# Performance work log

Measured on AMD Instinct MI355X. Metric: run time of the kernel, lower is better.

The kernel has to match this reference:

```python
import jax, jax.numpy as jnp
import numpy as np

B, C, P, T, H = 4, 256, 1024, 64, 8
D = C // H
SCALE = float(np.sqrt(D * T))


def setup_inputs() -> dict:
    key = jax.random.key(0)
    ks = jax.random.split(key, 7)
    s = 1.0 / np.sqrt(C)
    return {
        "x": jax.random.normal(ks[0], (B, C, P, T), dtype=jnp.float32),
        "Wk": jax.random.uniform(ks[1], (C, C), dtype=jnp.float32, minval=-s, maxval=s),
        "bk": jax.random.uniform(ks[2], (C,), dtype=jnp.float32, minval=-s, maxval=s),
        "Wq": jax.random.uniform(ks[3], (C, C), dtype=jnp.float32, minval=-s, maxval=s),
        "bq": jax.random.uniform(ks[4], (C,), dtype=jnp.float32, minval=-s, maxval=s),
        "Wv": jax.random.uniform(ks[5], (C, C), dtype=jnp.float32, minval=-s, maxval=s),
        "bv": jax.random.uniform(ks[6], (C,), dtype=jnp.float32, minval=-s, maxval=s),
    }


def _proj_split(x, W, b):
    # 1x1 conv == channel-mixing linear; then split heads: b (h d) p t -> b h d p t
    y = jnp.einsum('bcpt,oc->bopt', x, W) + b[None, :, None, None]
    Bs, _, Ps, Ts = y.shape
    return y.reshape(Bs, H, D, Ps, Ts)


def reference(x, Wk, bk, Wq, bq, Wv, bv):
    k = _proj_split(x, Wk, bk)
    q = _proj_split(x, Wq, bq)
    v = _proj_split(x, Wv, bv)
    # contract jointly over d and t
    energy = jnp.einsum('bhdpt,bhdqt->bhpq', k, q)
    attn = jax.nn.softmax(energy / SCALE, axis=-1)
    out = jnp.einsum('bhpq,bhdpt->bhdqt', attn, v)
    # merge heads: b h d q t -> b (h d) q t
    return out.reshape(B, C, P, T)
```

## Files before the change

### kernel.cpp

```cpp
#include <hip/hip_runtime.h>
#include <cstdint>
#include <cstddef>

#define NB 4
#define NC 256
#define NP 1024
#define NT 64
#define NH 8
#define ND 32
#define NF 2048
#define NPT 65536
#define KQV_ELEMS 67108864ull
#define INV_SCALE 0.022097086912079608f

typedef unsigned short u16;
typedef __bf16 bf16x8 __attribute__((ext_vector_type(8)));
typedef short  s16x8  __attribute__((ext_vector_type(8)));
typedef short  s16x4  __attribute__((ext_vector_type(4)));
typedef float  f32x4  __attribute__((ext_vector_type(4)));

__device__ __forceinline__ u16 f2bf(float f) {
  unsigned u = __builtin_bit_cast(unsigned, f);
  u += 0x7fffu + ((u >> 16) & 1u);
  return (u16)(u >> 16);
}
__device__ __forceinline__ float bf2f(u16 h) {
  unsigned u = ((unsigned)h) << 16;
  return __builtin_bit_cast(float, u);
}
__device__ __forceinline__ int swz(int row) { return ((row ^ (row >> 3)) & 7) << 4; }

#define GLOAD_LDS16(gp, lp) __builtin_amdgcn_global_load_lds( \
    (const __attribute__((address_space(1))) void*)(gp),      \
    (__attribute__((address_space(3))) void*)(lp), 16, 0, 0)

__device__ __forceinline__ f32x4 mfma16(bf16x8 a, bf16x8 b, f32x4 c) {
  return __builtin_amdgcn_mfma_f32_16x16x32_bf16(a, b, c, 0, 0, 0);
}

__global__ __launch_bounds__(256) void wcast_kernel(
    const float* __restrict__ Wk, const float* __restrict__ Wq,
    const float* __restrict__ Wv, u16* __restrict__ wbf)
{
  int pj = blockIdx.y;
  const float* W = (pj == 0) ? Wk : ((pj == 1) ? Wq : Wv);
  int idx = blockIdx.x * 1024 + threadIdx.x * 4;
  float4 v = *(const float4*)(W + idx);
  s16x4 pk;
  pk[0] = (short)f2bf(v.x); pk[1] = (short)f2bf(v.y);
  pk[2] = (short)f2bf(v.z); pk[3] = (short)f2bf(v.w);
  *(s16x4*)(wbf + (size_t)pj * 65536 + idx) = pk;
}

__global__ __launch_bounds__(256, 2) void xcast_kernel(
    const float* __restrict__ x, u16* __restrict__ xT)
{
  int ptt = blockIdx.x;
  int ct  = blockIdx.y;
  int b   = blockIdx.z;
  __shared__ __align__(16) u16 L[64 * 64];
  int tid = threadIdx.x;
#pragma unroll
  for (int i = 0; i < 4; i++) {
    int cl  = i * 16 + (tid >> 4);
    int ptl = (tid & 15) * 4;
    float4 v = *(const float4*)(x + ((size_t)(b * NC + ct * 64 + cl)) * NPT +
                                ptt * 64 + ptl);
    s16x4 pk;
    pk[0] = (short)f2bf(v.x); pk[1] = (short)f2bf(v.y);
    pk[2] = (short)f2bf(v.z); pk[3] = (short)f2bf(v.w);
    *(s16x4*)((char*)L + ((cl * 128 + ptl * 2) ^ swz(cl))) = pk;
  }
  __syncthreads();
#pragma unroll
  for (int i = 0; i < 2; i++) {
    int ptl = i * 32 + (tid >> 3);
    int c8  = (tid & 7) * 8;
    s16x8 v;
#pragma unroll
    for (int j = 0; j < 8; j++) {
      int row = c8 + j;
      v[j] = (short)*(const u16*)((char*)L + ((row * 128 + ptl * 2) ^ swz(row)));
    }
    *(s16x8*)(xT + ((size_t)b * NPT + (size_t)ptt * 64 + ptl) * NC + ct * 64 + c8) = v;
  }
}

template <int KT>
__device__ __forceinline__ void gemm_core(const u16* __restrict__ A,
                                          const u16* __restrict__ Bp,
                                          u16* As, u16* Bs, f32x4 acc[4][4])
{
  const int tid = threadIdx.x, lane = tid & 63, wave = tid >> 6;
  const int wm = (wave >> 1) * 64, wn = (wave & 1) * 64;
  for (int ks = 0; ks < KT / 64; ks++) {
    const int k0 = ks * 64;
    __syncthreads();
#pragma unroll
    for (int i = 0; i < 4; i++) {
      int r0 = wave * 32 + i * 8;
      int row = r0 + (lane >> 3);
      int col = k0 + (lane & 7) * 8;
      GLOAD_LDS16(A  + (size_t)row * KT + col, &As[r0 * 64]);
      GLOAD_LDS16(Bp + (size_t)row * KT + col, &Bs[r0 * 64]);
    }
    __syncthreads();
#pragma unroll
    for (int kk = 0; kk < 2; kk++) {
      bf16x8 af[4], bfr[4];
#pragma unroll
      for (int f = 0; f < 4; f++) {
        int ra = wm + f * 16 + (lane & 15);
        af[f]  = *(const bf16x8*)((char*)As + ra * 128 + kk * 64 + (lane >> 4) * 16);
        int rb = wn + f * 16 + (lane & 15);
        bfr[f] = *(const bf16x8*)((char*)Bs + rb * 128 + kk * 64 + (lane >> 4) * 16);
      }
#pragma unroll
      for (int fm = 0; fm < 4; fm++)
#pragma unroll
        for (int fn = 0; fn < 4; fn++)
          acc[fm][fn] = mfma16(af[fm], bfr[fn], acc[fm][fn]);
    }
  }
}

__global__ __launch_bounds__(256, 2) void proj_kernel(
    const u16* __restrict__ wbf, const u16* __restrict__ xT,
    const float* __restrict__ bk, const float* __restrict__ bq,
    const float* __restrict__ bv, u16* __restrict__ kqv)
{
  int d0 = blockIdx.x;
  int b  = blockIdx.y;
  int xcd = d0 & 7, r = d0 >> 3;
  int j = r % 6, tch = r / 6;
  int ptile = tch * 8 + xcd;
  int pj = j >> 1, mt = j & 1;
  const float* bias = (pj == 0) ? bk : ((pj == 1) ? bq : bv);
  u16* outb = kqv + (size_t)pj * KQV_ELEMS;

  const int m0 = mt * 128;
  const int n0 = ptile * 128;

  const u16* A  = wbf + (size_t)pj * 65536 + (size_t)m0 * NC;
  const u16* Bp = xT + ((size_t)b * NPT + (size_t)n0) * NC;

  __shared__ __align__(16) u16 As[128 * 64];
  __shared__ __align__(16) u16 Bs[128 * 64];

  f32x4 acc[4][4];
#pragma unroll
  for (int a = 0; a < 4; a++)
#pragma unroll
    for (int c = 0; c < 4; c++) acc[a][c] = (f32x4){0.f, 0.f, 0.f, 0.f};

  gemm_core<NC>(A, Bp, As, Bs, acc);

  const int lane = threadIdx.x & 63, wave = threadIdx.x >> 6;
  const int wm = (wave >> 1) * 64, wn = (wave & 1) * 64;
#pragma unroll
  for (int fm = 0; fm < 4; fm++) {
#pragma unroll
    for (int jj = 0; jj < 4; jj++) {
      int m = wm + fm * 16 + (lane >> 4) * 4 + jj;
      int o = m0 + m;
      float bsv = bias[o];
      int hh = o >> 5, dd = o & 31;
#pragma unroll
      for (int fn = 0; fn < 4; fn++) {
        int n = n0 + wn + fn * 16 + (lane & 15);
        int p = n >> 6, t = n & 63;
        outb[((size_t)(b * NH + hh) * NP + p) * NF + dd * 64 + t] =
            f2bf(acc[fm][fn][jj] + bsv);
      }
    }
  }
}

__global__ __launch_bounds__(256, 2) void transpose_kernel(
    const u16* __restrict__ in, u16* __restrict__ outp)
{
  int ft = blockIdx.x;
  int pt = blockIdx.y;
  int slab = blockIdx.z;
  __shared__ __align__(16) u16 L[64 * 64];
  int t = threadIdx.x;
  const u16* ip = in + (size_t)slab * NP * NF;
#pragma unroll
  for (int i = 0; i < 2; i++) {
    int pl = i * 32 + (t >> 3);
    int c8 = (t & 7) * 8;
    s16x8 v = *(const s16x8*)(ip + (size_t)(pt * 64 + pl) * NF + ft * 64 + c8);
    *(s16x8*)((char*)L + ((pl * 128 + c8 * 2) ^ swz(pl))) = v;
  }
  __syncthreads();
  u16* op = outp + (size_t)slab * NP * NF;
#pragma unroll
  for (int i = 0; i < 2; i++) {
    int fl = i * 32 + (t >> 3);
    int p8 = (t & 7) * 8;
    s16x8 v;
#pragma unroll
    for (int j2 = 0; j2 < 8; j2++) {
      int row = p8 + j2;
      v[j2] = (short)*(const u16*)((char*)L + ((row * 128 + fl * 2) ^ swz(row)));
    }
    *(s16x8*)(op + (size_t)(ft * 64 + fl) * NP + pt * 64 + p8) = v;
  }
}

__global__ __launch_bounds__(256, 2) void qk_kernel(
    const u16* __restrict__ kb, const u16* __restrict__ qb, u16* __restrict__ S)
{
  int bid = blockIdx.x;
  int xcd = bid & 7, r = bid >> 3;
  int bh = xcd * 4 + (r >> 6);
  int idx = r & 63;
  int mt = idx >> 3, nt = idx & 7;

  const u16* A  = qb + (size_t)bh * NP * NF + (size_t)mt * 128 * NF;
  const u16* Bp = kb + (size_t)bh * NP * NF + (size_t)nt * 128 * NF;

  __shared__ __align__(16) u16 As[128 * 64];
  __shared__ __align__(16) u16 Bs[128 * 64];

  f32x4 acc[4][4];
#pragma unroll
  for (int a = 0; a < 4; a++)
#pragma unroll
    for (int c = 0; c < 4; c++) acc[a][c] = (f32x4){0.f, 0.f, 0.f, 0.f};

  gemm_core<NF>(A, Bp, As, Bs, acc);

  const int lane = threadIdx.x & 63, wave = threadIdx.x >> 6;
  const int wm = (wave >> 1) * 64, wn = (wave & 1) * 64;
  u16* Sp = S + (size_t)bh * NP * NP;
#pragma unroll
  for (int fm = 0; fm < 4; fm++)
#pragma unroll
    for (int jj = 0; jj < 4; jj++) {
      int m = mt * 128 + wm + fm * 16 + (lane >> 4) * 4 + jj;
#pragma unroll
      for (int fn = 0; fn < 4; fn++) {
        int n = nt * 128 + wn + fn * 16 + (lane & 15);
        Sp[(size_t)m * NP + n] = f2bf(acc[fm][fn][jj] * INV_SCALE);
      }
    }
}

__global__ __launch_bounds__(256, 2) void softmax_kernel(
    const u16* __restrict__ S, u16* __restrict__ A)
{
  int cb = blockIdx.x;
  int bh = blockIdx.y;
  int tid = threadIdx.x;
  int c  = tid & 63;
  int qs = tid >> 6;
  int col = cb * 64 + c;
  const u16* Sp = S + (size_t)bh * NP * NP + col;
  float m = -1e30f, l = 0.f;
  for (int q = qs * 256; q < qs * 256 + 256; q++) {
    float v = bf2f(Sp[(size_t)q * NP]);
    float mn = fmaxf(m, v);
    l = l * __expf(m - mn) + __expf(v - mn);
    m = mn;
  }
  __shared__ float ms[4][64], ls[4][64];
  ms[qs][c] = m; ls[qs][c] = l;
  __syncthreads();
  float M = fmaxf(fmaxf(ms[0][c], ms[1][c]), fmaxf(ms[2][c], ms[3][c]));
  float L = ls[0][c] * __expf(ms[0][c] - M) + ls[1][c] * __expf(ms[1][c] - M) +
            ls[2][c] * __expf(ms[2][c] - M) + ls[3][c] * __expf(ms[3][c] - M);
  float inv = 1.f / L;
  u16* Ap = A + (size_t)bh * NP * NP + col;
  for (int q = qs * 256; q < qs * 256 + 256; q++) {
    float v = bf2f(Sp[(size_t)q * NP]);
    Ap[(size_t)q * NP] = f2bf(__expf(v - M) * inv);
  }
}

__global__ __launch_bounds__(256, 2) void av_kernel(
    const u16* __restrict__ Ab, const u16* __restrict__ Vt, float* __restrict__ out)
{
  int bid = blockIdx.x;
  int xcd = bid & 7, r = bid >> 3;
  int bh = xcd * 4 + (r >> 7);
  int idx = r & 127;
  int mt = idx >> 4, nt = idx & 15;

  const u16* A  = Ab + (size_t)bh * NP * NP + (size_t)mt * 128 * NP;
  const u16* Bp = Vt + (size_t)bh * NF * NP + (size_t)nt * 128 * NP;

  __shared__ __align__(16) u16 As[128 * 64];
  __shared__ __align__(16) u16 Bs[128 * 64];

  f32x4 acc[4][4];
#pragma unroll
  for (int a = 0; a < 4; a++)
#pragma unroll
    for (int c = 0; c < 4; c++) acc[a][c] = (f32x4){0.f, 0.f, 0.f, 0.f};

  gemm_core<NP>(A, Bp, As, Bs, acc);

  const int lane = threadIdx.x & 63, wave = threadIdx.x >> 6;
  const int wm = (wave >> 1) * 64, wn = (wave & 1) * 64;
  int b = bh >> 3, h = bh & 7;
#pragma unroll
  for (int fm = 0; fm < 4; fm++)
#pragma unroll
    for (int jj = 0; jj < 4; jj++) {
      int m = mt * 128 + wm + fm * 16 + (lane >> 4) * 4 + jj;
#pragma unroll
      for (int fn = 0; fn < 4; fn++) {
        int n = nt * 128 + wn + fn * 16 + (lane & 15);
        int dd = n >> 6, t = n & 63;
        out[((size_t)(b * NC + h * ND + dd) * NP + m) * NT + t] = acc[fm][fn][jj];
      }
    }
}

extern "C" void kernel_launch(void* const* d_in, const int* in_sizes, int n_in,
                              void* d_out, int out_size, void* d_ws, size_t ws_size,
                              hipStream_t stream)
{
  if (ws_size < 4ull * KQV_ELEMS * sizeof(u16)) return;

  const float* x  = (const float*)d_in[0];
  const float* Wk = (const float*)d_in[1];
  const float* bk = (const float*)d_in[2];
  const float* Wq = (const float*)d_in[3];
  const float* bq = (const float*)d_in[4];
  const float* Wv = (const float*)d_in[5];
  const float* bv = (const float*)d_in[6];

  u16* kb = (u16*)d_ws;
  u16* qb = kb + KQV_ELEMS;
  u16* vb = kb + 2 * KQV_ELEMS;
  u16* vt = kb + 3 * KQV_ELEMS;

  u16* xT  = (u16*)d_out;
  u16* wbf = xT + KQV_ELEMS;
  u16* Sb  = xT + KQV_ELEMS + 262144;
  u16* Ab  = kb;

  wcast_kernel<<<dim3(64, 3), 256, 0, stream>>>(Wk, Wq, Wv, wbf);
  xcast_kernel<<<dim3(1024, 4, 4), 256, 0, stream>>>(x, xT);
  proj_kernel<<<dim3(3072, 4), 256, 0, stream>>>(wbf, xT, bk, bq, bv, kb);
  transpose_kernel<<<dim3(32, 16, 32), 256, 0, stream>>>(vb, vt);
  qk_kernel<<<dim3(2048), 256, 0, stream>>>(kb, qb, Sb);
  softmax_kernel<<<dim3(16, 32), 256, 0, stream>>>(Sb, Ab);
  av_kernel<<<dim3(4096), 256, 0, stream>>>(Ab, vt, (float*)d_out);
}
```

Baseline: 765.2 us.

## Double-buffer LDS tiles in projection GEMM to overlap loads with MFMA

Replaces the shared gemm_core call in the QKV projection kernel with an inlined K loop that uses two LDS buffers per operand. The next 64-wide K slice is issued via direct global-to-LDS loads while MFMAs run on the current slice, with explicit vmcnt waits and barriers. This aims to hide global load latency behind compute, at the cost of doubling the LDS footprint to 64 KB, which may reduce occupancy.

```diff
diff --git a/kernel.cpp b/kernel.cpp
--- a/kernel.cpp
+++ b/kernel.cpp
@@ -144,8 +144,13 @@
   const u16* A  = wbf + (size_t)pj * 65536 + (size_t)m0 * NC;
   const u16* Bp = xT + ((size_t)b * NPT + (size_t)n0) * NC;
 
-  __shared__ __align__(16) u16 As[128 * 64];
-  __shared__ __align__(16) u16 Bs[128 * 64];
+  __shared__ __align__(16) u16 As[2][128 * 64];
+  __shared__ __align__(16) u16 Bs[2][128 * 64];
+
+  const int tid  = threadIdx.x;
+  const int lane = tid & 63;
+  const int wave = tid >> 6;
+  const int wm = (wave >> 1) * 64, wn = (wave & 1) * 64;
 
   f32x4 acc[4][4];
 #pragma unroll
@@ -153,10 +158,54 @@
 #pragma unroll
     for (int c = 0; c < 4; c++) acc[a][c] = (f32x4){0.f, 0.f, 0.f, 0.f};
 
-  gemm_core<NC>(A, Bp, As, Bs, acc);
-
-  const int lane = threadIdx.x & 63, wave = threadIdx.x >> 6;
-  const int wm = (wave >> 1) * 64, wn = (wave & 1) * 64;
+  auto STAGE = [&](int pb, int k0) {
+#pragma unroll
+    for (int i = 0; i < 4; i++) {
+      int r0 = wave * 32 + i * 8;
+      int row = r0 + (lane >> 3);
+      int col = k0 + (lane & 7) * 8;
+      GLOAD_LDS16(A  + (size_t)row * NC + col, &As[pb][r0 * 64]);
+      GLOAD_LDS16(Bp + (size_t)row * NC + col, &Bs[pb][r0 * 64]);
+    }
+  };
+
+  STAGE(0, 0);
+  __builtin_amdgcn_sched_barrier(0);
+#pragma unroll
+  for (int ks = 0; ks < 4; ks++) {
+    if (ks < 3) {
+      STAGE((ks + 1) & 1, (ks + 1) * 64);
+      __builtin_amdgcn_sched_barrier(0);
+      asm volatile("s_waitcnt vmcnt(8)" ::: "memory");
+    } else {
+      asm volatile("s_waitcnt vmcnt(0)" ::: "memory");
+    }
+    __builtin_amdgcn_s_barrier();
+    __builtin_amdgcn_sched_barrier(0);
+    const u16* Asb = As[ks & 1];
+    const u16* Bsb = Bs[ks & 1];
+#pragma unroll
+    for (int kk = 0; kk < 2; kk++) {
+      bf16x8 af[4], bfr[4];
+#pragma unroll
+      for (int f = 0; f < 4; f++) {
+        int ra = wm + f * 16 + (lane & 15);
+        af[f]  = *(const bf16x8*)((char*)Asb + ra * 128 + kk * 64 + (lane >> 4) * 16);
+        int rb = wn + f * 16 + (lane & 15);
+        bfr[f] = *(const bf16x8*)((char*)Bsb + rb * 128 + kk * 64 + (lane >> 4) * 16);
+      }
+#pragma unroll
+      for (int fm = 0; fm < 4; fm++)
+#pragma unroll
+        for (int fn = 0; fn < 4; fn++)
+          acc[fm][fn] = mfma16(af[fm], bfr[fn], acc[fm][fn]);
+    }
+    __builtin_amdgcn_sched_barrier(0);
+    asm volatile("s_waitcnt lgkmcnt(0)" ::: "memory");
+    __builtin_amdgcn_s_barrier();
+    __builtin_amdgcn_sched_barrier(0);
+  }
+
 #pragma unroll
   for (int fm = 0; fm < 4; fm++) {
 #pragma unroll
```

Result: slower. 814.2 us (+6.4%).

## Replace QK and AV GEMMs with 256x256-tile, 4-stage pipelined 512-thread kernels

Applied to the files above, without the earlier changes.

Swaps the 128x128-tile QK^T and attn·V GEMM kernels for a new core that computes 256x256 tiles with 8 waves. Operands are staged through a 4-deep ring of LDS buffers using direct global-to-LDS loads, explicit vmcnt waits and barriers, and raised wave priority around the MFMA blocks. The larger tiles are meant to cut global/L2 traffic per FLOP, and the deeper prefetch is meant to hide memory latency. The cost is 128 KB of dynamic LDS per block, much higher register pressure from 32 accumulators per thread, and fewer blocks per CU.

```diff
diff --git a/kernel.cpp b/kernel.cpp
--- a/kernel.cpp
+++ b/kernel.cpp
@@ -208,41 +208,176 @@
   }
 }
 
-__global__ __launch_bounds__(256, 2) void qk_kernel(
+#define STG1(TT, I, OP) do {                                                   \
+    const u16* gp_ = (OP ? Bg : Ag) + (size_t)grow[I] * KT + (TT) * 32 + gcol[I]; \
+    GLOAD_LDS16(gp_, L + ((((TT) & 3) * 32768 + (OP) * 16384 +                 \
+                           ((I) & 1 ? W1 : W0)) >> 1));                        \
+  } while (0)
+
+#define FENCE() do {                                                           \
+    asm volatile("" ::: "memory");                                             \
+    __builtin_amdgcn_sched_barrier(0);                                         \
+  } while (0)
+
+#define KBODY(J, WAITASM, DOSTG) do {                                          \
+    const int bufb_ = ((J) & 3) * 32768;                                       \
+    bf16x8 a_[4], b_[4];                                                       \
+    _Pragma("unroll")                                                          \
+    for (int mf = 0; mf < 4; mf++)                                             \
+      a_[mf] = *(const bf16x8*)((const char*)L + bufb_ + baseA + mf * 1024);   \
+    _Pragma("unroll")                                                          \
+    for (int nf = 0; nf < 4; nf++)                                             \
+      b_[nf] = *(const bf16x8*)((const char*)L + bufb_ + baseB + nf * 1024);   \
+    if (DOSTG) { STG1((J) + 3, 0, 0); STG1((J) + 3, 1, 0); }                   \
+    __builtin_amdgcn_s_barrier();                                              \
+    asm volatile("s_waitcnt lgkmcnt(0)" ::: "memory");                         \
+    __builtin_amdgcn_sched_barrier(0);                                         \
+    __builtin_amdgcn_s_setprio(1);                                             \
+    _Pragma("unroll")                                                          \
+    for (int mf = 0; mf < 4; mf++)                                             \
+      _Pragma("unroll")                                                        \
+      for (int nf = 0; nf < 4; nf++)                                           \
+        acc[mf][nf] = mfma16(a_[mf], b_[nf], acc[mf][nf]);                     \
+    __builtin_amdgcn_s_setprio(0);                                             \
+    __builtin_amdgcn_sched_barrier(0);                                         \
+    __builtin_amdgcn_s_barrier();                                              \
+    FENCE();                                                                   \
+    bf16x8 a2_[4];                                                             \
+    _Pragma("unroll")                                                          \
+    for (int mf = 0; mf < 4; mf++)                                             \
+      a2_[mf] = *(const bf16x8*)((const char*)L + bufb_ + baseA +              \
+                                 (4 + mf) * 1024);                             \
+    if (DOSTG) { STG1((J) + 3, 2, 1); STG1((J) + 3, 3, 1); }                   \
+    __builtin_amdgcn_s_barrier();                                              \
+    asm volatile("s_waitcnt lgkmcnt(0)" ::: "memory");                         \
+    __builtin_amdgcn_sched_barrier(0);                                         \
+    __builtin_amdgcn_s_setprio(1);                                             \
+    _Pragma("unroll")                                                          \
+    for (int mf = 0; mf < 4; mf++)                                             \
+      _Pragma("unroll")                                                        \
+      for (int nf = 0; nf < 4; nf++)                                           \
+        acc[4 + mf][nf] = mfma16(a2_[mf], b_[nf], acc[4 + mf][nf]);            \
+    __builtin_amdgcn_s_setprio(0);                                             \
+    __builtin_amdgcn_sched_barrier(0);                                         \
+    asm volatile(WAITASM ::: "memory");                                        \
+    __builtin_amdgcn_s_barrier();                                              \
+    FENCE();                                                                   \
+  } while (0)
+
+template <int KT>
+__device__ __forceinline__ void core256(const u16* __restrict__ Ag,
+                                        const u16* __restrict__ Bg,
+                                        u16* L, f32x4 acc[8][4])
+{
+  constexpr int NKT = KT / 32;
+  const int tid  = threadIdx.x;
+  const int lane = tid & 63;
+  const int wv   = tid >> 6;
+  const int wr = wv >> 2, wc = wv & 3;
+
+  int grow[4], gcol[4];
+#pragma unroll
+  for (int i = 0; i < 4; i++) {
+    int oi   = (tid + (i & 1) * 512) * 16;
+    int loff = oi ^ (((oi >> 6) & 3) << 4);
+    grow[i] = loff >> 6;
+    gcol[i] = (loff & 63) >> 1;
+  }
+  const int W0 = wv * 1024;
+  const int W1 = wv * 1024 + 8192;
+
+  const int rowA  = wr * 128 + (lane & 15);
+  const int baseA = rowA * 64 + (((lane >> 4) * 16) ^ ((rowA & 3) << 4));
+  const int rowB  = wc * 64 + (lane & 15);
+  const int baseB = 16384 + rowB * 64 + (((lane >> 4) * 16) ^ ((rowB & 3) << 4));
+
+#pragma unroll
+  for (int tt = 0; tt < 3; tt++) {
+    STG1(tt, 0, 0); STG1(tt, 1, 0); STG1(tt, 2, 1); STG1(tt, 3, 1);
+  }
+  __builtin_amdgcn_sched_barrier(0);
+  asm volatile("s_waitcnt vmcnt(8)" ::: "memory");
+  __builtin_amdgcn_s_barrier();
+  FENCE();
+
+  for (int j = 0; j < NKT - 3; ++j)
+    KBODY(j, "s_waitcnt vmcnt(8)", 1);
+  KBODY(NKT - 3, "s_waitcnt vmcnt(4)", 0);
+  KBODY(NKT - 2, "s_waitcnt vmcnt(0)", 0);
+  KBODY(NKT - 1, "", 0);
+}
+
+__global__ __launch_bounds__(512, 2) void qk256_kernel(
     const u16* __restrict__ kb, const u16* __restrict__ qb, u16* __restrict__ S)
 {
+  extern __shared__ u16 L[];
   int bid = blockIdx.x;
   int xcd = bid & 7, r = bid >> 3;
-  int bh = xcd * 4 + (r >> 6);
-  int idx = r & 63;
-  int mt = idx >> 3, nt = idx & 7;
-
-  const u16* A  = qb + (size_t)bh * NP * NF + (size_t)mt * 128 * NF;
-  const u16* Bp = kb + (size_t)bh * NP * NF + (size_t)nt * 128 * NF;
-
-  __shared__ __align__(16) u16 As[128 * 64];
-  __shared__ __align__(16) u16 Bs[128 * 64];
-
-  f32x4 acc[4][4];
-#pragma unroll
-  for (int a = 0; a < 4; a++)
+  int bh  = xcd * 4 + (r >> 4);
+  int til = r & 15;
+  int mt  = til >> 2, nt = til & 3;
+
+  const u16* Ag = qb + (size_t)bh * NP * NF + (size_t)mt * 256 * NF;
+  const u16* Bg = kb + (size_t)bh * NP * NF + (size_t)nt * 256 * NF;
+
+  f32x4 acc[8][4];
+#pragma unroll
+  for (int a = 0; a < 8; a++)
 #pragma unroll
     for (int c = 0; c < 4; c++) acc[a][c] = (f32x4){0.f, 0.f, 0.f, 0.f};
 
-  gemm_core<NF>(A, Bp, As, Bs, acc);
-
-  const int lane = threadIdx.x & 63, wave = threadIdx.x >> 6;
-  const int wm = (wave >> 1) * 64, wn = (wave & 1) * 64;
+  core256<NF>(Ag, Bg, L, acc);
+
+  const int lane = threadIdx.x & 63, wv = threadIdx.x >> 6;
+  const int wr = wv >> 2, wc = wv & 3;
   u16* Sp = S + (size_t)bh * NP * NP;
 #pragma unroll
-  for (int fm = 0; fm < 4; fm++)
+  for (int mf = 0; mf < 8; mf++)
 #pragma unroll
     for (int jj = 0; jj < 4; jj++) {
-      int m = mt * 128 + wm + fm * 16 + (lane >> 4) * 4 + jj;
-#pragma unroll
-      for (int fn = 0; fn < 4; fn++) {
-        int n = nt * 128 + wn + fn * 16 + (lane & 15);
-        Sp[(size_t)m * NP + n] = f2bf(acc[fm][fn][jj] * INV_SCALE);
+      int m = mt * 256 + wr * 128 + mf * 16 + (lane >> 4) * 4 + jj;
+#pragma unroll
+      for (int nf = 0; nf < 4; nf++) {
+        int n = nt * 256 + wc * 64 + nf * 16 + (lane & 15);
+        Sp[(size_t)m * NP + n] = f2bf(acc[mf][nf][jj] * INV_SCALE);
+      }
+    }
+}
+
+__global__ __launch_bounds__(512, 2) void av256_kernel(
+    const u16* __restrict__ Ab, const u16* __restrict__ Vt, float* __restrict__ out)
+{
+  extern __shared__ u16 L[];
+  int bid = blockIdx.x;
+  int xcd = bid & 7, r = bid >> 3;
+  int bh  = xcd * 4 + (r >> 5);
+  int til = r & 31;
+  int mt  = til >> 3, ntf = til & 7;
+
+  const u16* Ag = Ab + (size_t)bh * NP * NP + (size_t)mt * 256 * NP;
+  const u16* Bg = Vt + (size_t)bh * NF * NP + (size_t)ntf * 256 * NP;
+
+  f32x4 acc[8][4];
+#pragma unroll
+  for (int a = 0; a < 8; a++)
+#pragma unroll
+    for (int c = 0; c < 4; c++) acc[a][c] = (f32x4){0.f, 0.f, 0.f, 0.f};
+
+  core256<NP>(Ag, Bg, L, acc);
+
+  const int lane = threadIdx.x & 63, wv = threadIdx.x >> 6;
+  const int wr = wv >> 2, wc = wv & 3;
+  int b = bh >> 3, h = bh & 7;
+#pragma unroll
+  for (int mf = 0; mf < 8; mf++)
+#pragma unroll
+    for (int jj = 0; jj < 4; jj++) {
+      int m = mt * 256 + wr * 128 + mf * 16 + (lane >> 4) * 4 + jj;
+#pragma unroll
+      for (int nf = 0; nf < 4; nf++) {
+        int n = ntf * 256 + wc * 64 + nf * 16 + (lane & 15);
+        int dd = n >> 6, t = n & 63;
+        out[((size_t)(b * NC + h * ND + dd) * NP + m) * NT + t] = acc[mf][nf][jj];
       }
     }
 }
@@ -278,46 +413,6 @@
   }
 }
 
-__global__ __launch_bounds__(256, 2) void av_kernel(
-    const u16* __restrict__ Ab, const u16* __restrict__ Vt, float* __restrict__ out)
-{
-  int bid = blockIdx.x;
-  int xcd = bid & 7, r = bid >> 3;
-  int bh = xcd * 4 + (r >> 7);
-  int idx = r & 127;
-  int mt = idx >> 4, nt = idx & 15;
-
-  const u16* A  = Ab + (size_t)bh * NP * NP + (size_t)mt * 128 * NP;
-  const u16* Bp = Vt + (size_t)bh * NF * NP + (size_t)nt * 128 * NP;
-
-  __shared__ __align__(16) u16 As[128 * 64];
-  __shared__ __align__(16) u16 Bs[128 * 64];
-
-  f32x4 acc[4][4];
-#pragma unroll
-  for (int a = 0; a < 4; a++)
-#pragma unroll
-    for (int c = 0; c < 4; c++) acc[a][c] = (f32x4){0.f, 0.f, 0.f, 0.f};
-
-  gemm_core<NP>(A, Bp, As, Bs, acc);
-
-  const int lane = threadIdx.x & 63, wave = threadIdx.x >> 6;
-  const int wm = (wave >> 1) * 64, wn = (wave & 1) * 64;
-  int b = bh >> 3, h = bh & 7;
-#pragma unroll
-  for (int fm = 0; fm < 4; fm++)
-#pragma unroll
-    for (int jj = 0; jj < 4; jj++) {
-      int m = mt * 128 + wm + fm * 16 + (lane >> 4) * 4 + jj;
-#pragma unroll
-      for (int fn = 0; fn < 4; fn++) {
-        int n = nt * 128 + wn + fn * 16 + (lane & 15);
-        int dd = n >> 6, t = n & 63;
-        out[((size_t)(b * NC + h * ND + dd) * NP + m) * NT + t] = acc[fm][fn][jj];
-      }
-    }
-}
-
 extern "C" void kernel_launch(void* const* d_in, const int* in_sizes, int n_in,
                               void* d_out, int out_size, void* d_ws, size_t ws_size,
                               hipStream_t stream)
@@ -342,11 +437,16 @@
   u16* Sb  = xT + KQV_ELEMS + 262144;
   u16* Ab  = kb;
 
+  (void)hipFuncSetAttribute((const void*)qk256_kernel,
+                            hipFuncAttributeMaxDynamicSharedMemorySize, 131072);
+  (void)hipFuncSetAttribute((const void*)av256_kernel,
+                            hipFuncAttributeMaxDynamicSharedMemorySize, 131072);
+
   wcast_kernel<<<dim3(64, 3), 256, 0, stream>>>(Wk, Wq, Wv, wbf);
   xcast_kernel<<<dim3(1024, 4, 4), 256, 0, stream>>>(x, xT);
   proj_kernel<<<dim3(3072, 4), 256, 0, stream>>>(wbf, xT, bk, bq, bv, kb);
   transpose_kernel<<<dim3(32, 16, 32), 256, 0, stream>>>(vb, vt);
-  qk_kernel<<<dim3(2048), 256, 0, stream>>>(kb, qb, Sb);
+  qk256_kernel<<<dim3(512), 512, 131072, stream>>>(kb, qb, Sb);
   softmax_kernel<<<dim3(16, 32), 256, 0, stream>>>(Sb, Ab);
-  av_kernel<<<dim3(4096), 256, 0, stream>>>(Ab, vt, (float*)d_out);
-}
+  av256_kernel<<<dim3(1024), 512, 131072, stream>>>(Ab, vt, (float*)d_out);
+}
```

After: 719.0 us. 6.0% less time.
